# Kernel tuning notes

Hardware: AMD Instinct MI355X
Metric: run time of the kernel (lower is better)

Reference implementation:

```python
import jax, jax.numpy as jnp
import numpy as np

B = 16384; HB = 120; BD = 9; NS = 32; NF = 15  # history_bars, bar_descr, n_skills, n_forecast


def _lin_attn(x, wq, wk, wv, wo, bo, g, b):
    # x: [N, S, D_in]; linear attention with phi = elu + 1, residual + LayerNorm
    phi = lambda z: jax.nn.elu(z) + 1.0
    Q = phi(jnp.einsum('nsd,ed->nse', x, wq))
    K = phi(jnp.einsum('nsd,ed->nse', x, wk))
    V = jnp.einsum('nsd,ed->nse', x, wv)
    kv = jnp.einsum('nsd,nse->nde', K, V)              # [N, D, D]
    num = jnp.einsum('nsd,nde->nse', Q, kv)
    den = jnp.maximum(jnp.sum(Q * jnp.sum(K, axis=1, keepdims=True), axis=-1, keepdims=True), 1e-6)
    o = num / den
    y = jnp.einsum('nse,fe->nsf', o, wo) + bo + o      # out_proj + residual
    mu = jnp.mean(y, axis=-1, keepdims=True)
    var = jnp.var(y, axis=-1, keepdims=True)
    return (y - mu) * jax.lax.rsqrt(var + 1e-5) * g + b


def _forward(x, bn_g, bn_b, bn_m, bn_v, wq2, wk2, wv2, wo2, bo2, ln2g, ln2b,
             wq4, wk4, wv4, wo4, bo4, ln4g, ln4b,
             w_ih, w_hh, b_ih, b_hh, cg_w, cg_uw, cg_ub,
             w6, b6, w7, b7, rev_w, rev_b):
    Bn = x.shape[0]
    # BatchNorm1d (eval mode, running stats)
    out = (x - bn_m) * jax.lax.rsqrt(bn_v + 1e-5) * bn_g + bn_b
    # lin_attn_2: tokens = 120 time steps, d = 9 variables
    out = _lin_attn(out.reshape(Bn, HB, BD), wq2, wk2, wv2, wo2, bo2, ln2g, ln2b)
    # transpose_3: [B, 120, 9] -> [B, 9, 120]
    out = jnp.transpose(out, (0, 2, 1))
    # lin_attn_4: 9 parallel sequences of one 120-dim token
    out = _lin_attn(out.reshape(Bn * BD, 1, HB), wq4, wk4, wv4, wo4, bo4, ln4g, ln4b)
    # CGLSTM over 120 steps, vectorized across (batch * 9 variables)
    xs = jnp.transpose(out.reshape(Bn * BD, HB, 1), (1, 0, 2))  # [120, B*9, 1]
    h0 = jnp.zeros((Bn * BD, NS), x.dtype)

    def step(carry, x_t):
        h, c = carry
        gates = x_t @ w_ih.T + b_ih + h @ w_hh.T + b_hh  # [N, 4*NS]
        i, f, g, o = jnp.split(gates, 4, axis=-1)         # torch LSTMCell gate order
        c_new = jax.nn.sigmoid(f) * c + jax.nn.sigmoid(i) * jnp.tanh(g)
        gc = jax.nn.sigmoid(x_t @ cg_w.T + h @ cg_uw.T + cg_ub)  # contextual gate uses old h
        h_new = gc * jnp.tanh(c_new)                      # LSTM's own h output is discarded
        return (h_new, c_new), None

    (h, _), _ = jax.lax.scan(step, (h0, h0), xs)
    cglstm_out = h.reshape(Bn, BD * NS)                   # [B, 288]
    # conv_6 (pointwise per variable) + softplus, conv_7 + tanh
    t = jax.nn.softplus(h @ w6.T + b6)                    # [B*9, 60]
    t = jnp.tanh(t @ w7.T + b7).reshape(Bn, NF * BD)      # [B, 135]
    # transpose_8: view [B,15,9] -> [B,9,15]
    y = jnp.transpose(t.reshape(Bn, NF, BD), (0, 2, 1)).reshape(Bn, -1)
    # RevIN (normalize over full 135-dim vector, unbiased std as in torch.std)
    mu = jnp.mean(y, axis=-1, keepdims=True)
    sd = jnp.maximum(jnp.std(y, axis=-1, keepdims=True, ddof=1), 1e-5)
    enc = (y - mu) / sd * rev_w + rev_b
    return cglstm_out, enc


def setup_inputs() -> dict:
    key = jax.random.key(0)
    ks = jax.random.split(key, 20)
    r = lambda i, s, sc=0.1: jax.random.normal(ks[i], s, jnp.float32) * sc
    return dict(
        x=jax.random.normal(ks[0], (B, HB * BD), jnp.float32),
        bn_g=jnp.ones((HB * BD,), jnp.float32), bn_b=jnp.zeros((HB * BD,), jnp.float32),
        bn_m=r(1, (HB * BD,)),
        bn_v=jax.random.uniform(ks[2], (HB * BD,), jnp.float32, 0.5, 1.5),
        wq2=r(3, (BD, BD), 0.3), wk2=r(4, (BD, BD), 0.3), wv2=r(5, (BD, BD), 0.3),
        wo2=r(6, (BD, BD), 0.3), bo2=jnp.zeros((BD,), jnp.float32),
        ln2g=jnp.ones((BD,), jnp.float32), ln2b=jnp.zeros((BD,), jnp.float32),
        wq4=r(7, (HB, HB), 0.05), wk4=r(8, (HB, HB), 0.05), wv4=r(9, (HB, HB), 0.05),
        wo4=r(10, (HB, HB), 0.05), bo4=jnp.zeros((HB,), jnp.float32),
        ln4g=jnp.ones((HB,), jnp.float32), ln4b=jnp.zeros((HB,), jnp.float32),
        w_ih=r(11, (4 * NS, 1), 0.2), w_hh=r(12, (4 * NS, NS), 0.1),
        b_ih=jnp.zeros((4 * NS,), jnp.float32), b_hh=jnp.zeros((4 * NS,), jnp.float32),
        cg_w=r(13, (NS, 1), 0.2), cg_uw=r(14, (NS, NS), 0.1), cg_ub=jnp.zeros((NS,), jnp.float32),
        w6=r(15, (4 * NF, NS), 0.15), b6=jnp.zeros((4 * NF,), jnp.float32),
        w7=r(16, (NF, 4 * NF), 0.15), b7=jnp.zeros((NF,), jnp.float32),
        rev_w=jnp.ones((BD * NF,), jnp.float32), rev_b=jnp.zeros((BD * NF,), jnp.float32),
    )


def reference(x, bn_g, bn_b, bn_m, bn_v, wq2, wk2, wv2, wo2, bo2, ln2g, ln2b,
              wq4, wk4, wv4, wo4, bo4, ln4g, ln4b,
              w_ih, w_hh, b_ih, b_hh, cg_w, cg_uw, cg_ub,
              w6, b6, w7, b7, rev_w, rev_b):
    return _forward(x, bn_g, bn_b, bn_m, bn_v, wq2, wk2, wv2, wo2, bo2, ln2g, ln2b,
                    wq4, wk4, wv4, wo4, bo4, ln4g, ln4b,
                    w_ih, w_hh, b_ih, b_hh, cg_w, cg_uw, cg_ub,
                    w6, b6, w7, b7, rev_w, rev_b)
```

## Files before the change

### kernel.cpp

```cpp
#include <hip/hip_runtime.h>
#include <math.h>

#define NTH 256
#define SB 4

typedef __attribute__((ext_vector_type(8))) short bf16x8;
typedef __attribute__((ext_vector_type(4))) float f32x4;

__device__ __forceinline__ float fast_sigmoid(float x) {
    return __builtin_amdgcn_rcpf(1.0f + __expf(-x));
}
__device__ __forceinline__ float fast_tanh(float x) {
    return fmaf(-2.0f, __builtin_amdgcn_rcpf(__expf(2.0f * x) + 1.0f), 1.0f);
}
__device__ __forceinline__ short f2bf(float x) {
    unsigned u = __float_as_uint(x);
    return (short)((u + 0x7FFFu + ((u >> 16) & 1u)) >> 16);
}

extern "C" __global__ void __launch_bounds__(NTH, 3)
se_kernel(const float* __restrict__ x,
          const float* __restrict__ bn_g, const float* __restrict__ bn_b,
          const float* __restrict__ bn_m, const float* __restrict__ bn_v,
          const float* __restrict__ wq2, const float* __restrict__ wk2,
          const float* __restrict__ wv2, const float* __restrict__ wo2,
          const float* __restrict__ bo2, const float* __restrict__ ln2g,
          const float* __restrict__ ln2b,
          const float* __restrict__ wq4, const float* __restrict__ wk4,
          const float* __restrict__ wv4, const float* __restrict__ wo4,
          const float* __restrict__ bo4, const float* __restrict__ ln4g,
          const float* __restrict__ ln4b,
          const float* __restrict__ w_ih, const float* __restrict__ w_hh,
          const float* __restrict__ b_ih, const float* __restrict__ b_hh,
          const float* __restrict__ cg_w, const float* __restrict__ cg_uw,
          const float* __restrict__ cg_ub,
          const float* __restrict__ w6, const float* __restrict__ b6,
          const float* __restrict__ w7, const float* __restrict__ b7,
          const float* __restrict__ rev_w, const float* __restrict__ rev_b,
          float* __restrict__ out, int Bn)
{
    __shared__ __align__(16) float sm[9108];
    const int tid  = threadIdx.x;
    const int lane = tid & 63;
    const int wv   = tid >> 6;
    const int b0   = blockIdx.x * SB;
    const int nsamp = min(SB, Bn - b0);

    float* sU  = sm;
    float* SCR = sm + 4320;
    float* sWQ2 = sm + 8640; float* sWK2 = sm + 8724;
    float* sWV2 = sm + 8808; float* sWO2 = sm + 8892;
    float* sBO2 = sm + 8976; float* sLN2G = sm + 8988; float* sLN2B = sm + 9000;
    float* sKV = sm + 9012; float* sKS = sm + 9096;
    float* sBO4 = sm + 8640; float* sLN4G = sm + 8760; float* sLN4B = sm + 8880;
    float* sMU = sm + 9000; float* sRS = sm + 9020;
    float* sST = sm + 9040;
    float* sH0 = SCR;
    float* sH1 = SCR + 2112;
    float* sT1 = sU;
    float* sTF = sU + 2160;

    for (int i = tid; i < 81; i += NTH) {
        sWQ2[i] = wq2[i]; sWK2[i] = wk2[i]; sWV2[i] = wv2[i]; sWO2[i] = wo2[i];
    }
    if (tid < 9) { sBO2[tid] = bo2[tid]; sLN2G[tid] = ln2g[tid]; sLN2B[tid] = ln2b[tid]; }
    __syncthreads();

    float* S0 = SCR; float* S1 = SCR + 1080; float* S2 = SCR + 2160; float* S3 = SCR + 3240;
    for (int ss = 0; ss < SB; ++ss) {
        if (ss < nsamp) {
            const int b = b0 + ss;
            for (int i = tid; i < 1080; i += NTH) {
                float xv = x[(size_t)b * 1080 + i];
                S0[i] = (xv - bn_m[i]) * rsqrtf(bn_v[i] + 1e-5f) * bn_g[i] + bn_b[i];
            }
            __syncthreads();
            for (int idx = tid; idx < 1080; idx += NTH) {
                int s = idx / 9, e = idx - s * 9;
                float aq = 0.f, ak = 0.f, av = 0.f;
                #pragma unroll
                for (int d = 0; d < 9; ++d) {
                    float xv = S0[s * 9 + d];
                    aq = fmaf(xv, sWQ2[e * 9 + d], aq);
                    ak = fmaf(xv, sWK2[e * 9 + d], ak);
                    av = fmaf(xv, sWV2[e * 9 + d], av);
                }
                S1[idx] = aq >= 0.f ? aq + 1.f : __expf(aq);
                S2[idx] = ak >= 0.f ? ak + 1.f : __expf(ak);
                S3[idx] = av;
            }
            __syncthreads();
            if (tid < 81) {
                int d = tid / 9, e = tid - d * 9;
                float acc = 0.f;
                for (int s = 0; s < 120; ++s) acc = fmaf(S2[s * 9 + d], S3[s * 9 + e], acc);
                sKV[tid] = acc;
            } else if (tid < 90) {
                int d = tid - 81;
                float acc = 0.f;
                for (int s = 0; s < 120; ++s) acc += S2[s * 9 + d];
                sKS[d] = acc;
            }
            __syncthreads();
            for (int idx = tid; idx < 1080; idx += NTH) {
                int s = idx / 9, e = idx - s * 9;
                float num = 0.f, den = 0.f;
                #pragma unroll
                for (int d = 0; d < 9; ++d) {
                    float qv = S1[s * 9 + d];
                    num = fmaf(qv, sKV[d * 9 + e], num);
                    den = fmaf(qv, sKS[d], den);
                }
                S0[idx] = num / fmaxf(den, 1e-6f);
            }
            __syncthreads();
            for (int idx = tid; idx < 1080; idx += NTH) {
                int s = idx / 9, f = idx - s * 9;
                float acc = sBO2[f] + S0[s * 9 + f];
                #pragma unroll
                for (int e = 0; e < 9; ++e) acc = fmaf(S0[s * 9 + e], sWO2[f * 9 + e], acc);
                S1[idx] = acc;
            }
            __syncthreads();
            if (tid < 120) {
                int s = tid;
                float sum = 0.f, sq = 0.f;
                #pragma unroll
                for (int f = 0; f < 9; ++f) { float v = S1[s * 9 + f]; sum += v; sq = fmaf(v, v, sq); }
                float mu = sum * (1.f / 9.f);
                float rs = rsqrtf(sq * (1.f / 9.f) - mu * mu + 1e-5f);
                #pragma unroll
                for (int f = 0; f < 9; ++f)
                    sU[(ss * 9 + f) * 120 + s] = (S1[s * 9 + f] - mu) * rs * sLN2G[f] + sLN2B[f];
            }
        }
        __syncthreads();
    }

    for (int i = tid; i < 120; i += NTH) { sBO4[i] = bo4[i]; sLN4G[i] = ln4g[i]; sLN4B[i] = ln4b[i]; }
    for (int p = 0; p < 2; ++p) {
        float* V0 = SCR;
        float* Y0 = SCR + 2160;
        if (tid < 120) {
            int sp = tid / 60, ep = tid - sp * 60;
            int e0 = ep * 2;
            const float* uB = sU + (p * 2 + sp) * 1080;
            float acc[2][9];
            #pragma unroll
            for (int r = 0; r < 2; ++r)
                #pragma unroll
                for (int v = 0; v < 9; ++v) acc[r][v] = 0.f;
            const float* w0p = &wv4[e0 * 120];
            const float* w1p = &wv4[(e0 + 1) * 120];
            for (int dq = 0; dq < 30; ++dq) {
                float4 wA = *(const float4*)&w0p[dq * 4];
                float4 wB = *(const float4*)&w1p[dq * 4];
                #pragma unroll
                for (int v = 0; v < 9; ++v) {
                    float4 u = *(const float4*)&uB[v * 120 + dq * 4];
                    acc[0][v] = fmaf(wA.x, u.x, acc[0][v]); acc[0][v] = fmaf(wA.y, u.y, acc[0][v]);
                    acc[0][v] = fmaf(wA.z, u.z, acc[0][v]); acc[0][v] = fmaf(wA.w, u.w, acc[0][v]);
                    acc[1][v] = fmaf(wB.x, u.x, acc[1][v]); acc[1][v] = fmaf(wB.y, u.y, acc[1][v]);
                    acc[1][v] = fmaf(wB.z, u.z, acc[1][v]); acc[1][v] = fmaf(wB.w, u.w, acc[1][v]);
                }
            }
            float* dst = V0 + sp * 1080;
            #pragma unroll
            for (int v = 0; v < 9; ++v) {
                dst[v * 120 + e0]     = acc[0][v];
                dst[v * 120 + e0 + 1] = acc[1][v];
            }
        }
        __syncthreads();
        if (tid < 120) {
            int sp = tid / 60, ep = tid - sp * 60;
            int e0 = ep * 2;
            const float* vB = V0 + sp * 1080;
            float acc[2][9];
            #pragma unroll
            for (int r = 0; r < 2; ++r)
                #pragma unroll
                for (int v = 0; v < 9; ++v) acc[r][v] = 0.f;
            const float* w0p = &wo4[e0 * 120];
            const float* w1p = &wo4[(e0 + 1) * 120];
            for (int dq = 0; dq < 30; ++dq) {
                float4 wA = *(const float4*)&w0p[dq * 4];
                float4 wB = *(const float4*)&w1p[dq * 4];
                #pragma unroll
                for (int v = 0; v < 9; ++v) {
                    float4 u = *(const float4*)&vB[v * 120 + dq * 4];
                    acc[0][v] = fmaf(wA.x, u.x, acc[0][v]); acc[0][v] = fmaf(wA.y, u.y, acc[0][v]);
                    acc[0][v] = fmaf(wA.z, u.z, acc[0][v]); acc[0][v] = fmaf(wA.w, u.w, acc[0][v]);
                    acc[1][v] = fmaf(wB.x, u.x, acc[1][v]); acc[1][v] = fmaf(wB.y, u.y, acc[1][v]);
                    acc[1][v] = fmaf(wB.z, u.z, acc[1][v]); acc[1][v] = fmaf(wB.w, u.w, acc[1][v]);
                }
            }
            float* Y = Y0 + sp * 1080;
            #pragma unroll
            for (int v = 0; v < 9; ++v) {
                float o0 = vB[v * 120 + e0], o1 = vB[v * 120 + e0 + 1];
                Y[v * 120 + e0]     = acc[0][v] + sBO4[e0]     + o0;
                Y[v * 120 + e0 + 1] = acc[1][v] + sBO4[e0 + 1] + o1;
            }
        }
        __syncthreads();
        if (tid < 18) {
            int sp = tid / 9, v = tid - sp * 9;
            const float* Y = Y0 + sp * 1080 + v * 120;
            float sum = 0.f, sq = 0.f;
            for (int e = 0; e < 120; ++e) { float t = Y[e]; sum += t; sq = fmaf(t, t, sq); }
            float mu = sum * (1.f / 120.f);
            sMU[tid] = mu;
            sRS[tid] = rsqrtf(sq * (1.f / 120.f) - mu * mu + 1e-5f);
        }
        __syncthreads();
        for (int idx = tid; idx < 540; idx += NTH) {
            int sp = idx / 270, off = idx - sp * 270;
            int v = off / 30, qq = off - v * 30;
            const float* Y = Y0 + sp * 1080;
            float4 y = *(const float4*)&Y[v * 120 + qq * 4];
            float4 g = *(const float4*)&sLN4G[qq * 4];
            float4 bb = *(const float4*)&sLN4B[qq * 4];
            float mu = sMU[sp * 9 + v], rs = sRS[sp * 9 + v];
            float4 o;
            o.x = (y.x - mu) * rs * g.x + bb.x;
            o.y = (y.y - mu) * rs * g.y + bb.y;
            o.z = (y.z - mu) * rs * g.z + bb.z;
            o.w = (y.w - mu) * rs * g.w + bb.w;
            *(float4*)&sU[((p * 2 + sp) * 9 + v) * 120 + qq * 4] = o;
        }
        __syncthreads();
    }

    for (int i = tid; i < 2112; i += NTH) sH0[i] = 0.f;
    __syncthreads();

    const int c = lane & 15, q = lane >> 4;
    bf16x8 bfr[8]; float wxv[8], bsv[8];
    int grow[4] = {0, 0, 0, 0}; int pcol = 0;
    if (wv < 3) {
        bf16x8 pa, pb, pa2, pb2;
        #pragma unroll
        for (int j = 0; j < 8; ++j) { pa[j] = 0; pb[j] = 0; pa2[j] = 0; pb2[j] = 0; }
        if (q == 0) {
            pa[0]  = f2bf((float)c); pb[0]  = f2bf(1.0f);
            pa2[0] = f2bf(1.0f);     pb2[0] = f2bf((float)c);
        }
        f32x4 zc; zc[0] = zc[1] = zc[2] = zc[3] = 0.f;
        f32x4 prr = __builtin_amdgcn_mfma_f32_16x16x32_bf16(pa,  pb,  zc, 0, 0, 0);
        f32x4 pcc = __builtin_amdgcn_mfma_f32_16x16x32_bf16(pa2, pb2, zc, 0, 0, 0);
        #pragma unroll
        for (int r = 0; r < 4; ++r) grow[r] = wv * 16 + (int)(prr[r] + 0.5f);
        pcol = (int)(pcc[0] + 0.5f);

        #pragma unroll
        for (int T = 0; T < 8; ++T) {
            int gate = T >> 1, kk = ((T & 1) << 4) + pcol;
            const float* wr; float wx, bs;
            if (gate < 3) {
                int n = gate * 32 + kk;
                wr = &w_hh[n * 32]; wx = w_ih[n]; bs = b_ih[n] + b_hh[n];
            } else {
                wr = &cg_uw[kk * 32]; wx = cg_w[kk]; bs = cg_ub[kk];
            }
            bf16x8 tv;
            #pragma unroll
            for (int j = 0; j < 8; ++j) tv[j] = f2bf(wr[q * 8 + j]);
            bfr[T] = tv; wxv[T] = wx; bsv[T] = bs;
        }
    }
    float cst[8];
    #pragma unroll
    for (int i = 0; i < 8; ++i) cst[i] = 0.f;
    const int live9 = nsamp * 9;
    const float* ar0 = &sH0[(wv * 16 + c) * 44 + q * 8];
    const float* ar1 = &sH1[(wv * 16 + c) * 44 + q * 8];

#define LSTM_STEP(RP, WPL, XARR)                                               \
    if (wv < 3) {                                                              \
        float4 hA = *(const float4*)(RP);                                      \
        float4 hB = *(const float4*)((RP) + 4);                                \
        bf16x8 af;                                                             \
        af[0] = f2bf(hA.x); af[1] = f2bf(hA.y);                                \
        af[2] = f2bf(hA.z); af[3] = f2bf(hA.w);                                \
        af[4] = f2bf(hB.x); af[5] = f2bf(hB.y);                                \
        af[6] = f2bf(hB.z); af[7] = f2bf(hB.w);                                \
        f32x4 acc[8];                                                          \
        _Pragma("unroll")                                                      \
        for (int T = 0; T < 8; ++T) {                                          \
            f32x4 ci;                                                          \
            _Pragma("unroll")                                                  \
            for (int r = 0; r < 4; ++r) ci[r] = fmaf(wxv[T], XARR[r], bsv[T]); \
            acc[T] = __builtin_amdgcn_mfma_f32_16x16x32_bf16(af, bfr[T], ci, 0, 0, 0); \
        }                                                                      \
        _Pragma("unroll")                                                      \
        for (int kh = 0; kh < 2; ++kh) {                                       \
            _Pragma("unroll")                                                  \
            for (int r = 0; r < 4; ++r) {                                      \
                float si  = fast_sigmoid(acc[kh][r]);                          \
                float sf  = fast_sigmoid(acc[2 + kh][r]);                      \
                float tg  = fast_tanh(acc[4 + kh][r]);                         \
                float sgc = fast_sigmoid(acc[6 + kh][r]);                      \
                float cn = fmaf(sf, cst[kh * 4 + r], si * tg);                 \
                cst[kh * 4 + r] = cn;                                          \
                (WPL)[grow[r] * 44 + (kh << 4) + pcol] = sgc * fast_tanh(cn);  \
            }                                                                  \
        }                                                                      \
    }

    for (int t = 0; t < 120; t += 2) {
        float xa[4], xb[4];
        if (wv < 3) {
            #pragma unroll
            for (int r = 0; r < 4; ++r) {
                float2 xv;
                if (grow[r] < live9) xv = *(const float2*)&sU[grow[r] * 120 + t];
                else { xv.x = 0.f; xv.y = 0.f; }
                xa[r] = xv.x; xb[r] = xv.y;
            }
        }
        LSTM_STEP(ar0, sH1, xa)
        LSTM_STEP(ar1, sH0, xb)
    }
    __syncthreads();

    for (int idx = tid; idx < SB * 288; idx += NTH) {
        int ssd = idx / 288, r = idx - ssd * 288;
        if (ssd < nsamp) {
            int v = r >> 5, k = r & 31;
            out[(size_t)(b0 + ssd) * 288 + r] = sH0[(ssd * 9 + v) * 44 + k];
        }
    }

    for (int idx = tid; idx < SB * 540; idx += NTH) {
        int ssd = idx / 540, rem = idx - ssd * 540;
        int v = rem / 60, j = rem - v * 60;
        if (ssd < nsamp) {
            float acc = b6[j];
            const float4* wr4 = (const float4*)&w6[j * 32];
            const float4* hv = (const float4*)&sH0[(ssd * 9 + v) * 44];
            #pragma unroll
            for (int qq = 0; qq < 8; ++qq) {
                float4 w = wr4[qq], h = hv[qq];
                acc = fmaf(w.x, h.x, acc); acc = fmaf(w.y, h.y, acc);
                acc = fmaf(w.z, h.z, acc); acc = fmaf(w.w, h.w, acc);
            }
            sT1[idx] = acc > 15.f ? acc : log1pf(__expf(acc));
        }
    }
    __syncthreads();
    for (int idx = tid; idx < SB * 135; idx += NTH) {
        int ssd = idx / 135, rem = idx - ssd * 135;
        int v = rem / 15, f = rem - v * 15;
        if (ssd < nsamp) {
            float acc = b7[f];
            const float4* wr = (const float4*)&w7[f * 60];
            const float4* tv = (const float4*)&sT1[ssd * 540 + v * 60];
            #pragma unroll
            for (int qq = 0; qq < 15; ++qq) {
                float4 w = wr[qq], h = tv[qq];
                acc = fmaf(w.x, h.x, acc); acc = fmaf(w.y, h.y, acc);
                acc = fmaf(w.z, h.z, acc); acc = fmaf(w.w, h.w, acc);
            }
            sTF[idx] = fast_tanh(acc);
        }
    }
    __syncthreads();
    if (tid < SB && tid < nsamp) {
        const float* tf = &sTF[tid * 135];
        float sum = 0.f;
        for (int i = 0; i < 135; ++i) sum += tf[i];
        float mu = sum * (1.f / 135.f);
        float sq = 0.f;
        for (int i = 0; i < 135; ++i) { float d = tf[i] - mu; sq = fmaf(d, d, sq); }
        float sd = sqrtf(sq * (1.f / 134.f));
        sST[tid * 2]     = mu;
        sST[tid * 2 + 1] = 1.f / fmaxf(sd, 1e-5f);
    }
    __syncthreads();
    const size_t encbase = (size_t)Bn * 288;
    for (int idx = tid; idx < SB * 135; idx += NTH) {
        int ssd = idx / 135, j = idx - ssd * 135;
        if (ssd < nsamp) {
            int qq = j / 15, pp = j - qq * 15;
            float val = (sTF[ssd * 135 + pp * 9 + qq] - sST[ssd * 2]) * sST[ssd * 2 + 1] * rev_w[j] + rev_b[j];
            out[encbase + (size_t)(b0 + ssd) * 135 + j] = val;
        }
    }
}

extern "C" void kernel_launch(void* const* d_in, const int* in_sizes, int n_in,
                              void* d_out, int out_size, void* d_ws, size_t ws_size,
                              hipStream_t stream) {
    const float* x    = (const float*)d_in[0];
    const float* bn_g = (const float*)d_in[1];
    const float* bn_b = (const float*)d_in[2];
    const float* bn_m = (const float*)d_in[3];
    const float* bn_v = (const float*)d_in[4];
    const float* wq2  = (const float*)d_in[5];
    const float* wk2  = (const float*)d_in[6];
    const float* wv2  = (const float*)d_in[7];
    const float* wo2  = (const float*)d_in[8];
    const float* bo2  = (const float*)d_in[9];
    const float* ln2g = (const float*)d_in[10];
    const float* ln2b = (const float*)d_in[11];
    const float* wq4  = (const float*)d_in[12];
    const float* wk4  = (const float*)d_in[13];
    const float* wv4  = (const float*)d_in[14];
    const float* wo4  = (const float*)d_in[15];
    const float* bo4  = (const float*)d_in[16];
    const float* ln4g = (const float*)d_in[17];
    const float* ln4b = (const float*)d_in[18];
    const float* w_ih = (const float*)d_in[19];
    const float* w_hh = (const float*)d_in[20];
    const float* b_ih = (const float*)d_in[21];
    const float* b_hh = (const float*)d_in[22];
    const float* cg_w = (const float*)d_in[23];
    const float* cg_uw= (const float*)d_in[24];
    const float* cg_ub= (const float*)d_in[25];
    const float* w6   = (const float*)d_in[26];
    const float* b6   = (const float*)d_in[27];
    const float* w7   = (const float*)d_in[28];
    const float* b7   = (const float*)d_in[29];
    const float* rev_w= (const float*)d_in[30];
    const float* rev_b= (const float*)d_in[31];

    int Bn = in_sizes[0] / 1080;
    int grid = (Bn + SB - 1) / SB;
    hipLaunchKernelGGL(se_kernel, dim3(grid), dim3(NTH), 0, stream,
                       x, bn_g, bn_b, bn_m, bn_v, wq2, wk2, wv2, wo2, bo2, ln2g, ln2b,
                       wq4, wk4, wv4, wo4, bo4, ln4g, ln4b,
                       w_ih, w_hh, b_ih, b_hh, cg_w, cg_uw, cg_ub,
                       w6, b6, w7, b7, rev_w, rev_b,
                       (float*)d_out, Bn);
}
```

Before: 1.642 ms.

## Raise samples per block to seven and use all four waves in LSTM

Increases samples per block from 4 to 7 so the 63 (sample,variable) LSTM rows fill four 16-row MFMA tiles, letting all four waves run the recurrence instead of three. It also gives the attention-4 projections one output row per thread over 240 threads, and grows and re-lays out shared memory to match. The larger LDS footprint may reduce blocks per CU, and the 120-step LSTM work per block grows.

Result: faster. 1.524 ms (-7.2%).

```diff
diff --git a/kernel.cpp b/kernel.cpp
--- a/kernel.cpp
+++ b/kernel.cpp
@@ -2,7 +2,7 @@
 #include <math.h>
 
 #define NTH 256
-#define SB 4
+#define SB 7
 
 typedef __attribute__((ext_vector_type(8))) short bf16x8;
 typedef __attribute__((ext_vector_type(4))) float f32x4;
@@ -39,7 +39,7 @@
           const float* __restrict__ rev_w, const float* __restrict__ rev_b,
           float* __restrict__ out, int Bn)
 {
-    __shared__ __align__(16) float sm[9108];
+    __shared__ __align__(16) float sm[13552];
     const int tid  = threadIdx.x;
     const int lane = tid & 63;
     const int wv   = tid >> 6;
@@ -47,18 +47,18 @@
     const int nsamp = min(SB, Bn - b0);
 
     float* sU  = sm;
-    float* SCR = sm + 4320;
-    float* sWQ2 = sm + 8640; float* sWK2 = sm + 8724;
-    float* sWV2 = sm + 8808; float* sWO2 = sm + 8892;
-    float* sBO2 = sm + 8976; float* sLN2G = sm + 8988; float* sLN2B = sm + 9000;
-    float* sKV = sm + 9012; float* sKS = sm + 9096;
-    float* sBO4 = sm + 8640; float* sLN4G = sm + 8760; float* sLN4B = sm + 8880;
-    float* sMU = sm + 9000; float* sRS = sm + 9020;
-    float* sST = sm + 9040;
+    float* SCR = sm + 7560;
+    float* sWQ2 = sm + 13192; float* sWK2 = sm + 13273;
+    float* sWV2 = sm + 13354; float* sWO2 = sm + 13435;
+    float* sBO2 = sm + 13516; float* sLN2G = sm + 13525; float* sLN2B = sm + 13534;
+    float* sKV = sm + 11880;  float* sKS = sm + 11961;
+    float* sBO4 = sm + 13192; float* sLN4G = sm + 13312; float* sLN4B = sm + 13432;
+    float* sMU = sm + 11880;  float* sRS = sm + 11900;
+    float* sST = sm + 11920;
     float* sH0 = SCR;
-    float* sH1 = SCR + 2112;
+    float* sH1 = SCR + 2816;
     float* sT1 = sU;
-    float* sTF = sU + 2160;
+    float* sTF = sU + 3780;
 
     for (int i = tid; i < 81; i += NTH) {
         sWQ2[i] = wq2[i]; sWK2[i] = wk2[i]; sWV2[i] = wv2[i]; sWO2[i] = wo2[i];
@@ -138,75 +138,56 @@
     }
 
     for (int i = tid; i < 120; i += NTH) { sBO4[i] = bo4[i]; sLN4G[i] = ln4g[i]; sLN4B[i] = ln4b[i]; }
-    for (int p = 0; p < 2; ++p) {
+    for (int p = 0; p < 4; ++p) {
         float* V0 = SCR;
         float* Y0 = SCR + 2160;
-        if (tid < 120) {
-            int sp = tid / 60, ep = tid - sp * 60;
-            int e0 = ep * 2;
-            const float* uB = sU + (p * 2 + sp) * 1080;
-            float acc[2][9];
-            #pragma unroll
-            for (int r = 0; r < 2; ++r)
-                #pragma unroll
-                for (int v = 0; v < 9; ++v) acc[r][v] = 0.f;
-            const float* w0p = &wv4[e0 * 120];
-            const float* w1p = &wv4[(e0 + 1) * 120];
+        const int sp = tid / 120, erow = tid - sp * 120;
+        const int smp = p * 2 + sp;
+        const bool act = (tid < 240) && (smp < SB);
+        if (act) {
+            const float* uB = sU + smp * 1080;
+            float acc[9];
+            #pragma unroll
+            for (int v = 0; v < 9; ++v) acc[v] = 0.f;
+            const float* w0p = &wv4[erow * 120];
             for (int dq = 0; dq < 30; ++dq) {
                 float4 wA = *(const float4*)&w0p[dq * 4];
-                float4 wB = *(const float4*)&w1p[dq * 4];
                 #pragma unroll
                 for (int v = 0; v < 9; ++v) {
                     float4 u = *(const float4*)&uB[v * 120 + dq * 4];
-                    acc[0][v] = fmaf(wA.x, u.x, acc[0][v]); acc[0][v] = fmaf(wA.y, u.y, acc[0][v]);
-                    acc[0][v] = fmaf(wA.z, u.z, acc[0][v]); acc[0][v] = fmaf(wA.w, u.w, acc[0][v]);
-                    acc[1][v] = fmaf(wB.x, u.x, acc[1][v]); acc[1][v] = fmaf(wB.y, u.y, acc[1][v]);
-                    acc[1][v] = fmaf(wB.z, u.z, acc[1][v]); acc[1][v] = fmaf(wB.w, u.w, acc[1][v]);
+                    acc[v] = fmaf(wA.x, u.x, acc[v]); acc[v] = fmaf(wA.y, u.y, acc[v]);
+                    acc[v] = fmaf(wA.z, u.z, acc[v]); acc[v] = fmaf(wA.w, u.w, acc[v]);
                 }
             }
             float* dst = V0 + sp * 1080;
             #pragma unroll
-            for (int v = 0; v < 9; ++v) {
-                dst[v * 120 + e0]     = acc[0][v];
-                dst[v * 120 + e0 + 1] = acc[1][v];
-            }
+            for (int v = 0; v < 9; ++v) dst[v * 120 + erow] = acc[v];
         }
         __syncthreads();
-        if (tid < 120) {
-            int sp = tid / 60, ep = tid - sp * 60;
-            int e0 = ep * 2;
+        if (act) {
             const float* vB = V0 + sp * 1080;
-            float acc[2][9];
-            #pragma unroll
-            for (int r = 0; r < 2; ++r)
-                #pragma unroll
-                for (int v = 0; v < 9; ++v) acc[r][v] = 0.f;
-            const float* w0p = &wo4[e0 * 120];
-            const float* w1p = &wo4[(e0 + 1) * 120];
+            float acc[9];
+            #pragma unroll
+            for (int v = 0; v < 9; ++v) acc[v] = 0.f;
+            const float* w0p = &wo4[erow * 120];
             for (int dq = 0; dq < 30; ++dq) {
                 float4 wA = *(const float4*)&w0p[dq * 4];
-                float4 wB = *(const float4*)&w1p[dq * 4];
                 #pragma unroll
                 for (int v = 0; v < 9; ++v) {
                     float4 u = *(const float4*)&vB[v * 120 + dq * 4];
-                    acc[0][v] = fmaf(wA.x, u.x, acc[0][v]); acc[0][v] = fmaf(wA.y, u.y, acc[0][v]);
-                    acc[0][v] = fmaf(wA.z, u.z, acc[0][v]); acc[0][v] = fmaf(wA.w, u.w, acc[0][v]);
-                    acc[1][v] = fmaf(wB.x, u.x, acc[1][v]); acc[1][v] = fmaf(wB.y, u.y, acc[1][v]);
-                    acc[1][v] = fmaf(wB.z, u.z, acc[1][v]); acc[1][v] = fmaf(wB.w, u.w, acc[1][v]);
+                    acc[v] = fmaf(wA.x, u.x, acc[v]); acc[v] = fmaf(wA.y, u.y, acc[v]);
+                    acc[v] = fmaf(wA.z, u.z, acc[v]); acc[v] = fmaf(wA.w, u.w, acc[v]);
                 }
             }
             float* Y = Y0 + sp * 1080;
             #pragma unroll
-            for (int v = 0; v < 9; ++v) {
-                float o0 = vB[v * 120 + e0], o1 = vB[v * 120 + e0 + 1];
-                Y[v * 120 + e0]     = acc[0][v] + sBO4[e0]     + o0;
-                Y[v * 120 + e0 + 1] = acc[1][v] + sBO4[e0 + 1] + o1;
-            }
+            for (int v = 0; v < 9; ++v)
+                Y[v * 120 + erow] = acc[v] + sBO4[erow] + vB[v * 120 + erow];
         }
         __syncthreads();
-        if (tid < 18) {
-            int sp = tid / 9, v = tid - sp * 9;
-            const float* Y = Y0 + sp * 1080 + v * 120;
+        if (tid < 18 && (p * 2 + tid / 9) < SB) {
+            int sp2 = tid / 9, v = tid - sp2 * 9;
+            const float* Y = Y0 + sp2 * 1080 + v * 120;
             float sum = 0.f, sq = 0.f;
             for (int e = 0; e < 120; ++e) { float t = Y[e]; sum += t; sq = fmaf(t, t, sq); }
             float mu = sum * (1.f / 120.f);
@@ -215,30 +196,33 @@
         }
         __syncthreads();
         for (int idx = tid; idx < 540; idx += NTH) {
-            int sp = idx / 270, off = idx - sp * 270;
+            int sp2 = idx / 270, off = idx - sp2 * 270;
+            int smp2 = p * 2 + sp2;
             int v = off / 30, qq = off - v * 30;
-            const float* Y = Y0 + sp * 1080;
-            float4 y = *(const float4*)&Y[v * 120 + qq * 4];
-            float4 g = *(const float4*)&sLN4G[qq * 4];
-            float4 bb = *(const float4*)&sLN4B[qq * 4];
-            float mu = sMU[sp * 9 + v], rs = sRS[sp * 9 + v];
-            float4 o;
-            o.x = (y.x - mu) * rs * g.x + bb.x;
-            o.y = (y.y - mu) * rs * g.y + bb.y;
-            o.z = (y.z - mu) * rs * g.z + bb.z;
-            o.w = (y.w - mu) * rs * g.w + bb.w;
-            *(float4*)&sU[((p * 2 + sp) * 9 + v) * 120 + qq * 4] = o;
+            if (smp2 < SB) {
+                const float* Y = Y0 + sp2 * 1080;
+                float4 y = *(const float4*)&Y[v * 120 + qq * 4];
+                float4 g = *(const float4*)&sLN4G[qq * 4];
+                float4 bb = *(const float4*)&sLN4B[qq * 4];
+                float mu = sMU[sp2 * 9 + v], rs = sRS[sp2 * 9 + v];
+                float4 o;
+                o.x = (y.x - mu) * rs * g.x + bb.x;
+                o.y = (y.y - mu) * rs * g.y + bb.y;
+                o.z = (y.z - mu) * rs * g.z + bb.z;
+                o.w = (y.w - mu) * rs * g.w + bb.w;
+                *(float4*)&sU[(smp2 * 9 + v) * 120 + qq * 4] = o;
+            }
         }
         __syncthreads();
     }
 
-    for (int i = tid; i < 2112; i += NTH) sH0[i] = 0.f;
+    for (int i = tid; i < 2816; i += NTH) sH0[i] = 0.f;
     __syncthreads();
 
     const int c = lane & 15, q = lane >> 4;
     bf16x8 bfr[8]; float wxv[8], bsv[8];
-    int grow[4] = {0, 0, 0, 0}; int pcol = 0;
-    if (wv < 3) {
+    int grow[4]; int pcol;
+    {
         bf16x8 pa, pb, pa2, pb2;
         #pragma unroll
         for (int j = 0; j < 8; ++j) { pa[j] = 0; pb[j] = 0; pa2[j] = 0; pb2[j] = 0; }
@@ -277,7 +261,7 @@
     const float* ar1 = &sH1[(wv * 16 + c) * 44 + q * 8];
 
 #define LSTM_STEP(RP, WPL, XARR)                                               \
-    if (wv < 3) {                                                              \
+    {                                                                          \
         float4 hA = *(const float4*)(RP);                                      \
         float4 hB = *(const float4*)((RP) + 4);                                \
         bf16x8 af;                                                             \
@@ -310,14 +294,12 @@
 
     for (int t = 0; t < 120; t += 2) {
         float xa[4], xb[4];
-        if (wv < 3) {
-            #pragma unroll
-            for (int r = 0; r < 4; ++r) {
-                float2 xv;
-                if (grow[r] < live9) xv = *(const float2*)&sU[grow[r] * 120 + t];
-                else { xv.x = 0.f; xv.y = 0.f; }
-                xa[r] = xv.x; xb[r] = xv.y;
-            }
+        #pragma unroll
+        for (int r = 0; r < 4; ++r) {
+            float2 xv;
+            if (grow[r] < live9) xv = *(const float2*)&sU[grow[r] * 120 + t];
+            else { xv.x = 0.f; xv.y = 0.f; }
+            xa[r] = xv.x; xb[r] = xv.y;
         }
         LSTM_STEP(ar0, sH1, xa)
         LSTM_STEP(ar1, sH0, xb)
```
